# Optimization experiments

Hardware: AMD Instinct MI355X
Metric: run time of the kernel (lower is better)

## Reference

```python
import jax, jax.numpy as jnp
import numpy as np

B, T, C, H = 8, 2048, 1024, 128

def setup_inputs() -> dict:
    key = jax.random.key(0)
    k1, k2, k3, k4 = jax.random.split(key, 4)
    x = jax.random.normal(k1, (B, T, C), dtype=jnp.float32)
    Wq = jax.random.normal(k2, (C, H), dtype=jnp.float32) * (C ** -0.5)
    Wk = jax.random.normal(k3, (C, H), dtype=jnp.float32) * (C ** -0.5)
    Wv = jax.random.normal(k4, (C, H), dtype=jnp.float32) * (C ** -0.5)
    return {"x": x, "Wq": Wq, "Wk": Wk, "Wv": Wv}

def reference(x, Wq, Wk, Wv):
    # x: [B,T,C]; projections (no bias)
    q = jnp.einsum('btc,ch->bth', x, Wq)
    k = jnp.einsum('btc,ch->bth', x, Wk)
    v = jnp.einsum('btc,ch->bth', x, Wv)
    # NOTE: original module has NO 1/sqrt(head_size) scaling
    scores = jnp.einsum('bth,bsh->bts', q, k)  # [B,T,T]
    t = scores.shape[1]
    causal = jnp.tril(jnp.ones((t, t), dtype=bool))
    scores = jnp.where(causal, scores, -jnp.inf)
    attn = jax.nn.softmax(scores, axis=-1)  # dropout is identity in eval
    out = jnp.einsum('bts,bsh->bth', attn, v)  # [B,T,H]
    return out
```

## Files before the change

### kernel.cpp

```cpp
#include <hip/hip_runtime.h>

typedef __bf16 bf16;
typedef _Float16 f16;
typedef f16 f16x4 __attribute__((ext_vector_type(4)));
typedef f16 f16x8 __attribute__((ext_vector_type(8)));
typedef float f32x4 __attribute__((ext_vector_type(4)));

#define MFMA_FP(a, b, c) __builtin_amdgcn_mfma_f32_16x16x32_f16((a), (b), (c), 0, 0, 0)

static constexpr int Bn = 8, T = 2048, C = 1024, H = 128;
static constexpr int M = Bn * T;

__device__ __forceinline__ void gll16(const void* g, void* l) {
  __builtin_amdgcn_global_load_lds(
      (const __attribute__((address_space(1))) unsigned int*)g,
      (__attribute__((address_space(3))) unsigned int*)l, 16, 0, 0);
}

__global__ __launch_bounds__(256) void kwt(const float* __restrict__ Wq,
                                           const float* __restrict__ Wk,
                                           const float* __restrict__ Wv,
                                           f16* __restrict__ wt) {
  __shared__ float tl[32][33];
  const int w = blockIdx.z;
  const float* src = (w == 0) ? Wq : (w == 1) ? Wk : Wv;
  f16* dh = wt + (size_t)w * H * C;
  const int k0 = blockIdx.x * 32, n0 = blockIdx.y * 32;
  const int tx = threadIdx.x & 31, ty = threadIdx.x >> 5;
  for (int i = ty; i < 32; i += 8) tl[i][tx] = src[(size_t)(k0 + i) * H + n0 + tx];
  __syncthreads();
  for (int i = ty; i < 32; i += 8)
    dh[(size_t)(n0 + i) * C + k0 + tx] = (f16)tl[tx][i];
}

__global__ __launch_bounds__(256) void proj_kernel(const float* __restrict__ x,
                                                   const f16* __restrict__ wt,
                                                   f16* __restrict__ qo,
                                                   f16* __restrict__ ko,
                                                   f16* __restrict__ vt) {
  __shared__ __align__(16) float As[64 * 64];
  __shared__ __align__(16) f16  Bs[128 * 64];
  const int tid = threadIdx.x;
  const int lane = tid & 63, g = lane >> 4, r16 = lane & 15;
  const int wave = tid >> 6, wr = wave >> 1, wc = wave & 1;
  const int m0 = blockIdx.x * 64;
  const int which = blockIdx.y;
  const f16* wh = wt + (size_t)which * H * C;

  int asrc[4], bsrc[4];
  int aldu[4], bldu[4];
#pragma unroll
  for (int i = 0; i < 4; ++i) {
    const int u = wave * 4 + i;
    const int ra = u * 4 + (lane >> 4);
    asrc[i] = (m0 + ra) * C + (((lane & 15) ^ (ra & 7)) << 2);
    aldu[i] = u * 256;
    const int rb = u * 8 + (lane >> 3);
    bsrc[i] = rb * C + (((lane & 7) ^ (rb & 7)) << 3);
    bldu[i] = u * 512;
  }

  f32x4 acc[2][4] = {};

#define ISSUE(K0)                                                  \
  _Pragma("unroll")                                                \
  for (int i = 0; i < 4; ++i) {                                    \
    gll16(&x[asrc[i] + (K0)], &As[aldu[i]]);                       \
    gll16(&wh[bsrc[i] + (K0)], &Bs[bldu[i]]);                      \
  }

  ISSUE(0);
  for (int k0 = 0; k0 < C; k0 += 64) {
    __syncthreads();
#pragma unroll
    for (int kb = 0; kb < 2; ++kb) {
      f16x8 af[2], bf[4];
#pragma unroll
      for (int mt = 0; mt < 2; ++mt) {
        const int r = wr * 32 + mt * 16 + r16;
        const int s = r & 7;
        const f32x4 a0 = *(const f32x4*)&As[r * 64 + (((kb * 8 + g * 2) ^ s) << 2)];
        const f32x4 a1 = *(const f32x4*)&As[r * 64 + (((kb * 8 + g * 2 + 1) ^ s) << 2)];
#pragma unroll
        for (int j = 0; j < 4; ++j) { af[mt][j] = (f16)a0[j]; af[mt][4 + j] = (f16)a1[j]; }
      }
#pragma unroll
      for (int nt = 0; nt < 4; ++nt) {
        const int r = wc * 64 + nt * 16 + r16;
        const int phys = (kb * 4 + g) ^ (r & 7);
        bf[nt] = *(const f16x8*)&Bs[r * 64 + phys * 8];
      }
#pragma unroll
      for (int mt = 0; mt < 2; ++mt)
#pragma unroll
        for (int nt = 0; nt < 4; ++nt)
          acc[mt][nt] = MFMA_FP(af[mt], bf[nt], acc[mt][nt]);
    }
    __syncthreads();
    if (k0 + 64 < C) ISSUE(k0 + 64);
  }
#undef ISSUE

  if (which < 2) {
    f16* dst = which ? ko : qo;
#pragma unroll
    for (int mt = 0; mt < 2; ++mt)
#pragma unroll
      for (int nt = 0; nt < 4; ++nt) {
        const int mb = m0 + wr * 32 + mt * 16 + g * 4;
        const int col = wc * 64 + nt * 16 + r16;
#pragma unroll
        for (int r = 0; r < 4; ++r)
          dst[(size_t)(mb + r) * H + col] = (f16)acc[mt][nt][r];
      }
  } else {
    const int b = m0 >> 11;
    const int tb0 = m0 & 2047;
    f16* vbase = vt + (size_t)b * H * T;
#pragma unroll
    for (int mt = 0; mt < 2; ++mt)
#pragma unroll
      for (int nt = 0; nt < 4; ++nt) {
        const int tib = tb0 + wr * 32 + mt * 16 + g * 4;
        const int h = wc * 64 + nt * 16 + r16;
        f16x4 pk;
#pragma unroll
        for (int r = 0; r < 4; ++r) pk[r] = (f16)acc[mt][nt][r];
        *(f16x4*)&vbase[(size_t)h * T + tib] = pk;
      }
  }
}

__global__ __launch_bounds__(256, 2) void attn_kernel(const f16* __restrict__ qp,
                                                      const f16* __restrict__ kp,
                                                      const f16* __restrict__ vp,
                                                      float* __restrict__ out,
                                                      f16* __restrict__ oS,
                                                      float* __restrict__ MLs) {
  __shared__ __align__(16) f16 KS[2][64 * 128];
  __shared__ __align__(16) f16 VS[2][128 * 64];
  __shared__ __align__(16) f16 Pl[4][16][72];

  const int tid = threadIdx.x, lane = tid & 63, wave = tid >> 6;
  const int g = lane >> 4, q15 = lane & 15;
  const int x7 = q15 & 7;
  const int bb = blockIdx.x;
  const int b = bb & 7;
  const int t2 = bb >> 3;
  const int qt = 31 - (t2 >> 1);
  const int par = t2 & 1;
  const int q0 = qt * 64;
  const int qrow = q0 + wave * 16 + q15;
  const int task = b * 32 + qt;

  const f16* qb = qp + (size_t)b * T * H;
  const f16* kb = kp + (size_t)b * T * H;
  const f16* vb = vp + (size_t)b * H * T;

  int koff[4], voff[4], lo[4];
#pragma unroll
  for (int i = 0; i < 4; ++i) {
    const int u = wave * 4 + i;
    const int rK = u * 4 + (lane >> 4);
    koff[i] = rK * H + (((lane & 15) ^ (rK & 7)) << 3);
    const int hV = u * 8 + (lane >> 3);
    voff[i] = hV * T + (((lane & 7) ^ (hV & 7)) << 3);
    lo[i] = u * 512 + lane * 8;
  }

  const int n = (qt >= par) ? ((qt - par) >> 1) + 1 : 0;

  f16x8 qf[4];
#pragma unroll
  for (int k4 = 0; k4 < 4; ++k4)
    qf[k4] = *(const f16x8*)&qb[(size_t)qrow * H + k4 * 32 + g * 8];

  f32x4 o[8] = {};
  float mrun = -1e30f, lrun = 0.f;

  f16x8 rk[4], rv[4];
#define LOADT(S0)                                                   \
  _Pragma("unroll")                                                 \
  for (int i = 0; i < 4; ++i) {                                     \
    rk[i] = *(const f16x8*)&kb[(size_t)(S0) * H + koff[i]];         \
    rv[i] = *(const f16x8*)&vb[(size_t)(S0) + voff[i]];             \
  }
#define WRITET(BUF)                                                 \
  _Pragma("unroll")                                                 \
  for (int i = 0; i < 4; ++i) {                                     \
    *(f16x8*)&KS[BUF][lo[i]] = rk[i];                               \
    *(f16x8*)&VS[BUF][lo[i]] = rv[i];                               \
  }

  if (n > 0) {
    LOADT(par * 64);
    WRITET(0);
    if (n > 1) LOADT(par * 64 + 128);

    for (int k = 0; k < n; ++k) {
      const int s0 = par * 64 + k * 128;
      const int cur = k & 1;
      __syncthreads();

      f32x4 sacc[4] = {};
#pragma unroll
      for (int mt = 0; mt < 4; ++mt) {
        const int row = mt * 16 + q15;
#pragma unroll
        for (int k4 = 0; k4 < 4; ++k4) {
          const int pch = (k4 * 4 + g) ^ (row & 7);
          const f16x8 kf = *(const f16x8*)&KS[cur][row * 128 + pch * 8];
          sacc[mt] = MFMA_FP(kf, qf[k4], sacc[mt]);
        }
      }
      if (k == n - 1) {
#pragma unroll
        for (int mt = 0; mt < 4; ++mt)
#pragma unroll
          for (int r = 0; r < 4; ++r)
            if (s0 + mt * 16 + g * 4 + r > qrow) sacc[mt][r] = -1e30f;
      }
      float tmax = -1e30f;
#pragma unroll
      for (int mt = 0; mt < 4; ++mt)
#pragma unroll
        for (int r = 0; r < 4; ++r) tmax = fmaxf(tmax, sacc[mt][r]);
      tmax = fmaxf(tmax, __shfl_xor(tmax, 16));
      tmax = fmaxf(tmax, __shfl_xor(tmax, 32));
      if (!__all(tmax <= mrun + 8.f)) {
        const float mnew = fmaxf(mrun, tmax);
        const float alpha = __expf(mrun - mnew);
        lrun *= alpha;
#pragma unroll
        for (int i = 0; i < 8; ++i) o[i] *= alpha;
        mrun = mnew;
      }
      float lt = 0.f;
#pragma unroll
      for (int mt = 0; mt < 4; ++mt) {
        f16x4 pk;
#pragma unroll
        for (int r = 0; r < 4; ++r) {
          const float p = __expf(sacc[mt][r] - mrun);
          lt += p;
          pk[r] = (f16)p;
        }
        *(f16x4*)&Pl[wave][q15][mt * 16 + g * 4] = pk;
      }
      lt += __shfl_xor(lt, 16);
      lt += __shfl_xor(lt, 32);
      lrun += lt;
      const f16x8 pf0 = *(const f16x8*)&Pl[wave][q15][g * 8];
      const f16x8 pf1 = *(const f16x8*)&Pl[wave][q15][32 + g * 8];
#pragma unroll
      for (int mt = 0; mt < 8; ++mt) {
        const int h = mt * 16 + q15;
        const f16x8 vf0 = *(const f16x8*)&VS[cur][h * 64 + ((g ^ x7) << 3)];
        o[mt] = MFMA_FP(vf0, pf0, o[mt]);
        const f16x8 vf1 = *(const f16x8*)&VS[cur][h * 64 + (((4 + g) ^ x7) << 3)];
        o[mt] = MFMA_FP(vf1, pf1, o[mt]);
      }

      if (k + 1 < n) {
        WRITET(cur ^ 1);
        if (k + 2 < n) LOADT(par * 64 + (k + 2) * 128);
      }
    }
  }
#undef LOADT
#undef WRITET

  const float inv = (lrun > 0.f) ? 1.0f / lrun : 0.f;
  if (lane < 16) {
    MLs[((size_t)(task * 2 + par) * 64 + wave * 16 + lane) * 2 + 0] = mrun;
    MLs[((size_t)(task * 2 + par) * 64 + wave * 16 + lane) * 2 + 1] = lrun;
  }
  if (par == 0) {
    float* ob = out + ((size_t)b * T + qrow) * H;
#pragma unroll
    for (int mt = 0; mt < 8; ++mt) {
      f32x4 pk;
#pragma unroll
      for (int r = 0; r < 4; ++r) pk[r] = o[mt][r] * inv;
      *(f32x4*)&ob[mt * 16 + g * 4] = pk;
    }
  } else {
    f16* sb = oS + ((size_t)task * 64 + wave * 16 + q15) * 128;
#pragma unroll
    for (int mt = 0; mt < 8; ++mt) {
      f16x4 pk;
#pragma unroll
      for (int r = 0; r < 4; ++r) pk[r] = (f16)(o[mt][r] * inv);
      *(f16x4*)&sb[mt * 16 + g * 4] = pk;
    }
  }
}

__global__ __launch_bounds__(256) void combine_kernel(float* __restrict__ out,
                                                      const f16* __restrict__ oS,
                                                      const float* __restrict__ MLs) {
  const int task = blockIdx.x;
  const int b = task >> 5, qt = task & 31;
  const int tid = threadIdx.x;
  const int row = tid >> 2;
  const int cb = (tid & 3) * 32;
  const float m0 = MLs[((size_t)(task * 2 + 0) * 64 + row) * 2 + 0];
  const float l0 = MLs[((size_t)(task * 2 + 0) * 64 + row) * 2 + 1];
  const float m1 = MLs[((size_t)(task * 2 + 1) * 64 + row) * 2 + 0];
  const float l1 = MLs[((size_t)(task * 2 + 1) * 64 + row) * 2 + 1];
  const float Mg = fmaxf(m0, m1);
  const float w0 = l0 * __expf(m0 - Mg);
  const float w1 = l1 * __expf(m1 - Mg);
  const float inv = 1.0f / (w0 + w1);
  float* orow = out + ((size_t)b * T + qt * 64 + row) * H + cb;
  const f16* srow = oS + ((size_t)task * 64 + row) * 128 + cb;
#pragma unroll
  for (int c = 0; c < 32; c += 8) {
    const f16x8 o1 = *(const f16x8*)&srow[c];
    f32x4 a0 = *(const f32x4*)&orow[c];
    f32x4 a1 = *(const f32x4*)&orow[c + 4];
    f32x4 r0, r1;
#pragma unroll
    for (int r = 0; r < 4; ++r) {
      r0[r] = (w0 * a0[r] + w1 * (float)o1[r]) * inv;
      r1[r] = (w0 * a1[r] + w1 * (float)o1[4 + r]) * inv;
    }
    *(f32x4*)&orow[c] = r0;
    *(f32x4*)&orow[c + 4] = r1;
  }
}

extern "C" void kernel_launch(void* const* d_in, const int* in_sizes, int n_in,
                              void* d_out, int out_size, void* d_ws, size_t ws_size,
                              hipStream_t stream) {
  const float* x  = (const float*)d_in[0];
  const float* Wq = (const float*)d_in[1];
  const float* Wk = (const float*)d_in[2];
  const float* Wv = (const float*)d_in[3];
  float* out = (float*)d_out;

  f16*  wt  = (f16*)d_ws;
  f16*  qf  = wt + (size_t)3 * H * C;
  f16*  kf  = qf + (size_t)M * H;
  f16*  vf  = kf + (size_t)M * H;
  f16*  oS  = vf + (size_t)M * H;
  float* MLs = (float*)(oS + (size_t)256 * 64 * 128);

  kwt<<<dim3(C / 32, H / 32, 3), 256, 0, stream>>>(Wq, Wk, Wv, wt);
  proj_kernel<<<dim3(M / 64, 3), 256, 0, stream>>>(x, wt, qf, kf, vf);
  attn_kernel<<<512, 256, 0, stream>>>(qf, kf, vf, out, oS, MLs);
  combine_kernel<<<256, 256, 0, stream>>>(out, oS, MLs);
}
```

Measured before the change: 65.49 us.

## Use 128-row query tiles with 8 waves and 4-way KV split

The attention kernel now runs 512-thread blocks with eight waves covering 128 query rows, so each K/V tile loaded into LDS is shared by twice as many query rows. Work is split four ways over the key range instead of two, and the combine kernel merges four partial results. The LDS double buffer is replaced by a single buffer with register prefetch and two barriers per iteration. Waves skip fully masked tiles. The aim is to cut K/V load traffic per query and keep occupancy, at the cost of more sync stalls, more partial-output traffic and a heavier combine step.

```diff
diff --git a/kernel.cpp b/kernel.cpp
--- a/kernel.cpp
+++ b/kernel.cpp
@@ -131,15 +131,15 @@
   }
 }
 
-__global__ __launch_bounds__(256, 2) void attn_kernel(const f16* __restrict__ qp,
+__global__ __launch_bounds__(512, 4) void attn_kernel(const f16* __restrict__ qp,
                                                       const f16* __restrict__ kp,
                                                       const f16* __restrict__ vp,
                                                       float* __restrict__ out,
                                                       f16* __restrict__ oS,
                                                       float* __restrict__ MLs) {
-  __shared__ __align__(16) f16 KS[2][64 * 128];
-  __shared__ __align__(16) f16 VS[2][128 * 64];
-  __shared__ __align__(16) f16 Pl[4][16][72];
+  __shared__ __align__(16) f16 KS[64 * 128];
+  __shared__ __align__(16) f16 VS[128 * 64];
+  __shared__ __align__(16) f16 Pl[8][16][72];
 
   const int tid = threadIdx.x, lane = tid & 63, wave = tid >> 6;
   const int g = lane >> 4, q15 = lane & 15;
@@ -147,20 +147,22 @@
   const int bb = blockIdx.x;
   const int b = bb & 7;
   const int t2 = bb >> 3;
-  const int qt = 31 - (t2 >> 1);
-  const int par = t2 & 1;
-  const int q0 = qt * 64;
+  const int qt = (t2 < 32) ? (15 - (t2 >> 2)) : ((t2 - 32) >> 2);
+  const int par = t2 & 3;
+  const int q0 = qt * 128;
   const int qrow = q0 + wave * 16 + q15;
-  const int task = b * 32 + qt;
+  const int task = b * 16 + qt;
+  const int jmax = 2 * qt + 1;
+  const int n = (jmax >= par) ? ((jmax - par) >> 2) + 1 : 0;
 
   const f16* qb = qp + (size_t)b * T * H;
   const f16* kb = kp + (size_t)b * T * H;
   const f16* vb = vp + (size_t)b * H * T;
 
-  int koff[4], voff[4], lo[4];
-#pragma unroll
-  for (int i = 0; i < 4; ++i) {
-    const int u = wave * 4 + i;
+  int koff[2], voff[2], lo[2];
+#pragma unroll
+  for (int i = 0; i < 2; ++i) {
+    const int u = wave * 2 + i;
     const int rK = u * 4 + (lane >> 4);
     koff[i] = rK * H + (((lane & 15) ^ (rK & 7)) << 3);
     const int hV = u * 8 + (lane >> 3);
@@ -168,8 +170,6 @@
     lo[i] = u * 512 + lane * 8;
   }
 
-  const int n = (qt >= par) ? ((qt - par) >> 1) + 1 : 0;
-
   f16x8 qf[4];
 #pragma unroll
   for (int k4 = 0; k4 < 4; ++k4)
@@ -178,92 +178,94 @@
   f32x4 o[8] = {};
   float mrun = -1e30f, lrun = 0.f;
 
-  f16x8 rk[4], rv[4];
+  f16x8 rk[2], rv[2];
 #define LOADT(S0)                                                   \
   _Pragma("unroll")                                                 \
-  for (int i = 0; i < 4; ++i) {                                     \
+  for (int i = 0; i < 2; ++i) {                                     \
     rk[i] = *(const f16x8*)&kb[(size_t)(S0) * H + koff[i]];         \
     rv[i] = *(const f16x8*)&vb[(size_t)(S0) + voff[i]];             \
   }
-#define WRITET(BUF)                                                 \
+#define WRITET()                                                    \
   _Pragma("unroll")                                                 \
-  for (int i = 0; i < 4; ++i) {                                     \
-    *(f16x8*)&KS[BUF][lo[i]] = rk[i];                               \
-    *(f16x8*)&VS[BUF][lo[i]] = rv[i];                               \
+  for (int i = 0; i < 2; ++i) {                                     \
+    *(f16x8*)&KS[lo[i]] = rk[i];                                    \
+    *(f16x8*)&VS[lo[i]] = rv[i];                                    \
   }
 
   if (n > 0) {
     LOADT(par * 64);
-    WRITET(0);
-    if (n > 1) LOADT(par * 64 + 128);
-
-    for (int k = 0; k < n; ++k) {
-      const int s0 = par * 64 + k * 128;
-      const int cur = k & 1;
-      __syncthreads();
-
-      f32x4 sacc[4] = {};
-#pragma unroll
-      for (int mt = 0; mt < 4; ++mt) {
-        const int row = mt * 16 + q15;
-#pragma unroll
-        for (int k4 = 0; k4 < 4; ++k4) {
-          const int pch = (k4 * 4 + g) ^ (row & 7);
-          const f16x8 kf = *(const f16x8*)&KS[cur][row * 128 + pch * 8];
-          sacc[mt] = MFMA_FP(kf, qf[k4], sacc[mt]);
-        }
-      }
-      if (k == n - 1) {
+    WRITET();
+    __syncthreads();
+
+    for (int kk = 0; kk < n; ++kk) {
+      const int s0 = (par + 4 * kk) * 64;
+      if (kk + 1 < n) LOADT(s0 + 256);
+
+      if (s0 <= q0 + wave * 16 + 15) {
+        f32x4 sacc[4] = {};
+#pragma unroll
+        for (int mt = 0; mt < 4; ++mt) {
+          const int row = mt * 16 + q15;
+#pragma unroll
+          for (int k4 = 0; k4 < 4; ++k4) {
+            const int pch = (k4 * 4 + g) ^ (row & 7);
+            const f16x8 kf = *(const f16x8*)&KS[row * 128 + pch * 8];
+            sacc[mt] = MFMA_FP(kf, qf[k4], sacc[mt]);
+          }
+        }
+        if (s0 + 63 > q0 + wave * 16) {
+#pragma unroll
+          for (int mt = 0; mt < 4; ++mt)
+#pragma unroll
+            for (int r = 0; r < 4; ++r)
+              if (s0 + mt * 16 + g * 4 + r > qrow) sacc[mt][r] = -1e30f;
+        }
+        float tmax = -1e30f;
 #pragma unroll
         for (int mt = 0; mt < 4; ++mt)
 #pragma unroll
-          for (int r = 0; r < 4; ++r)
-            if (s0 + mt * 16 + g * 4 + r > qrow) sacc[mt][r] = -1e30f;
-      }
-      float tmax = -1e30f;
-#pragma unroll
-      for (int mt = 0; mt < 4; ++mt)
-#pragma unroll
-        for (int r = 0; r < 4; ++r) tmax = fmaxf(tmax, sacc[mt][r]);
-      tmax = fmaxf(tmax, __shfl_xor(tmax, 16));
-      tmax = fmaxf(tmax, __shfl_xor(tmax, 32));
-      if (!__all(tmax <= mrun + 8.f)) {
-        const float mnew = fmaxf(mrun, tmax);
-        const float alpha = __expf(mrun - mnew);
-        lrun *= alpha;
-#pragma unroll
-        for (int i = 0; i < 8; ++i) o[i] *= alpha;
-        mrun = mnew;
-      }
-      float lt = 0.f;
-#pragma unroll
-      for (int mt = 0; mt < 4; ++mt) {
-        f16x4 pk;
-#pragma unroll
-        for (int r = 0; r < 4; ++r) {
-          const float p = __expf(sacc[mt][r] - mrun);
-          lt += p;
-          pk[r] = (f16)p;
-        }
-        *(f16x4*)&Pl[wave][q15][mt * 16 + g * 4] = pk;
-      }
-      lt += __shfl_xor(lt, 16);
-      lt += __shfl_xor(lt, 32);
-      lrun += lt;
-      const f16x8 pf0 = *(const f16x8*)&Pl[wave][q15][g * 8];
-      const f16x8 pf1 = *(const f16x8*)&Pl[wave][q15][32 + g * 8];
-#pragma unroll
-      for (int mt = 0; mt < 8; ++mt) {
-        const int h = mt * 16 + q15;
-        const f16x8 vf0 = *(const f16x8*)&VS[cur][h * 64 + ((g ^ x7) << 3)];
-        o[mt] = MFMA_FP(vf0, pf0, o[mt]);
-        const f16x8 vf1 = *(const f16x8*)&VS[cur][h * 64 + (((4 + g) ^ x7) << 3)];
-        o[mt] = MFMA_FP(vf1, pf1, o[mt]);
-      }
-
-      if (k + 1 < n) {
-        WRITET(cur ^ 1);
-        if (k + 2 < n) LOADT(par * 64 + (k + 2) * 128);
+          for (int r = 0; r < 4; ++r) tmax = fmaxf(tmax, sacc[mt][r]);
+        tmax = fmaxf(tmax, __shfl_xor(tmax, 16));
+        tmax = fmaxf(tmax, __shfl_xor(tmax, 32));
+        if (!__all(tmax <= mrun + 8.f)) {
+          const float mnew = fmaxf(mrun, tmax);
+          const float alpha = __expf(mrun - mnew);
+          lrun *= alpha;
+#pragma unroll
+          for (int i = 0; i < 8; ++i) o[i] *= alpha;
+          mrun = mnew;
+        }
+        float lt = 0.f;
+#pragma unroll
+        for (int mt = 0; mt < 4; ++mt) {
+          f16x4 pk;
+#pragma unroll
+          for (int r = 0; r < 4; ++r) {
+            const float p = __expf(sacc[mt][r] - mrun);
+            lt += p;
+            pk[r] = (f16)p;
+          }
+          *(f16x4*)&Pl[wave][q15][mt * 16 + g * 4] = pk;
+        }
+        lt += __shfl_xor(lt, 16);
+        lt += __shfl_xor(lt, 32);
+        lrun += lt;
+        const f16x8 pf0 = *(const f16x8*)&Pl[wave][q15][g * 8];
+        const f16x8 pf1 = *(const f16x8*)&Pl[wave][q15][32 + g * 8];
+#pragma unroll
+        for (int mt = 0; mt < 8; ++mt) {
+          const int h = mt * 16 + q15;
+          const f16x8 vf0 = *(const f16x8*)&VS[h * 64 + ((g ^ x7) << 3)];
+          o[mt] = MFMA_FP(vf0, pf0, o[mt]);
+          const f16x8 vf1 = *(const f16x8*)&VS[h * 64 + (((4 + g) ^ x7) << 3)];
+          o[mt] = MFMA_FP(vf1, pf1, o[mt]);
+        }
+      }
+
+      if (kk + 1 < n) {
+        __syncthreads();
+        WRITET();
+        __syncthreads();
       }
     }
   }
@@ -272,8 +274,8 @@
 
   const float inv = (lrun > 0.f) ? 1.0f / lrun : 0.f;
   if (lane < 16) {
-    MLs[((size_t)(task * 2 + par) * 64 + wave * 16 + lane) * 2 + 0] = mrun;
-    MLs[((size_t)(task * 2 + par) * 64 + wave * 16 + lane) * 2 + 1] = lrun;
+    MLs[((size_t)(task * 4 + par) * 128 + wave * 16 + lane) * 2 + 0] = mrun;
+    MLs[((size_t)(task * 4 + par) * 128 + wave * 16 + lane) * 2 + 1] = lrun;
   }
   if (par == 0) {
     float* ob = out + ((size_t)b * T + qrow) * H;
@@ -285,7 +287,7 @@
       *(f32x4*)&ob[mt * 16 + g * 4] = pk;
     }
   } else {
-    f16* sb = oS + ((size_t)task * 64 + wave * 16 + q15) * 128;
+    f16* sb = oS + ((size_t)(task * 3 + par - 1) * 128 + wave * 16 + q15) * 128;
 #pragma unroll
     for (int mt = 0; mt < 8; ++mt) {
       f16x4 pk;
@@ -300,30 +302,37 @@
                                                       const f16* __restrict__ oS,
                                                       const float* __restrict__ MLs) {
   const int task = blockIdx.x;
-  const int b = task >> 5, qt = task & 31;
+  const int b = task >> 4, qt = task & 15;
   const int tid = threadIdx.x;
-  const int row = tid >> 2;
-  const int cb = (tid & 3) * 32;
-  const float m0 = MLs[((size_t)(task * 2 + 0) * 64 + row) * 2 + 0];
-  const float l0 = MLs[((size_t)(task * 2 + 0) * 64 + row) * 2 + 1];
-  const float m1 = MLs[((size_t)(task * 2 + 1) * 64 + row) * 2 + 0];
-  const float l1 = MLs[((size_t)(task * 2 + 1) * 64 + row) * 2 + 1];
-  const float Mg = fmaxf(m0, m1);
-  const float w0 = l0 * __expf(m0 - Mg);
-  const float w1 = l1 * __expf(m1 - Mg);
-  const float inv = 1.0f / (w0 + w1);
-  float* orow = out + ((size_t)b * T + qt * 64 + row) * H + cb;
-  const f16* srow = oS + ((size_t)task * 64 + row) * 128 + cb;
-#pragma unroll
-  for (int c = 0; c < 32; c += 8) {
-    const f16x8 o1 = *(const f16x8*)&srow[c];
+  const int row = tid >> 1;
+  const int cb = (tid & 1) * 64;
+  float m[4], l[4];
+#pragma unroll
+  for (int p = 0; p < 4; ++p) {
+    m[p] = MLs[((size_t)(task * 4 + p) * 128 + row) * 2 + 0];
+    l[p] = MLs[((size_t)(task * 4 + p) * 128 + row) * 2 + 1];
+  }
+  const float Mg = fmaxf(fmaxf(m[0], m[1]), fmaxf(m[2], m[3]));
+  float w[4], sum = 0.f;
+#pragma unroll
+  for (int p = 0; p < 4; ++p) { w[p] = l[p] * __expf(m[p] - Mg); sum += w[p]; }
+  const float inv = 1.0f / sum;
+  float* orow = out + ((size_t)b * T + qt * 128 + row) * H + cb;
+  const f16* s1 = oS + ((size_t)(task * 3 + 0) * 128 + row) * 128 + cb;
+  const f16* s2 = oS + ((size_t)(task * 3 + 1) * 128 + row) * 128 + cb;
+  const f16* s3 = oS + ((size_t)(task * 3 + 2) * 128 + row) * 128 + cb;
+#pragma unroll
+  for (int c = 0; c < 64; c += 8) {
+    const f16x8 o1 = *(const f16x8*)&s1[c];
+    const f16x8 o2 = *(const f16x8*)&s2[c];
+    const f16x8 o3 = *(const f16x8*)&s3[c];
     f32x4 a0 = *(const f32x4*)&orow[c];
     f32x4 a1 = *(const f32x4*)&orow[c + 4];
     f32x4 r0, r1;
 #pragma unroll
     for (int r = 0; r < 4; ++r) {
-      r0[r] = (w0 * a0[r] + w1 * (float)o1[r]) * inv;
-      r1[r] = (w0 * a1[r] + w1 * (float)o1[4 + r]) * inv;
+      r0[r] = (w[0] * a0[r] + w[1] * (float)o1[r] + w[2] * (float)o2[r] + w[3] * (float)o3[r]) * inv;
+      r1[r] = (w[0] * a1[r] + w[1] * (float)o1[4 + r] + w[2] * (float)o2[4 + r] + w[3] * (float)o3[4 + r]) * inv;
     }
     *(f32x4*)&orow[c] = r0;
     *(f32x4*)&orow[c + 4] = r1;
@@ -344,10 +353,10 @@
   f16*  kf  = qf + (size_t)M * H;
   f16*  vf  = kf + (size_t)M * H;
   f16*  oS  = vf + (size_t)M * H;
-  float* MLs = (float*)(oS + (size_t)256 * 64 * 128);
+  float* MLs = (float*)(oS + (size_t)128 * 3 * 128 * 128);
 
   kwt<<<dim3(C / 32, H / 32, 3), 256, 0, stream>>>(Wq, Wk, Wv, wt);
   proj_kernel<<<dim3(M / 64, 3), 256, 0, stream>>>(x, wt, qf, kf, vf);
-  attn_kernel<<<512, 256, 0, stream>>>(qf, kf, vf, out, oS, MLs);
-  combine_kernel<<<256, 256, 0, stream>>>(out, oS, MLs);
-}
+  attn_kernel<<<512, 512, 0, stream>>>(qf, kf, vf, out, oS, MLs);
+  combine_kernel<<<128, 256, 0, stream>>>(out, oS, MLs);
+}
```

After: 70.16 us. 7.1% more time.
